# Performance work log

Hardware: AMD Instinct MI355X
Metric: run time of the kernel (lower is better)

Reference implementation:

```python
import jax, jax.numpy as jnp
import numpy as np

XYZ_MIN = jnp.array([-1.0, -1.0, -1.0], dtype=jnp.float32)
XYZ_MAX = jnp.array([1.0, 1.0, 1.0], dtype=jnp.float32)
ACT_SHIFT = float(np.log(1.0 / (1.0 - 1e-6) - 1.0))  # density bias shift
WS = 100  # world_size per axis for num_voxels=1024000 in [-1,1]^3
R, P = 4096, 128  # rays, points per ray


def grid_sample_3d(grid, xyz):
    """Trilinear grid_sample, align_corners=True, zeros padding.
    grid: [C, D, H, W] (D=z, H=y, W=x); xyz: [N, 3] world coords. Returns [N, C]."""
    C, D, H, W = grid.shape
    norm = (xyz - XYZ_MIN) / (XYZ_MAX - XYZ_MIN) * 2.0 - 1.0  # [-1,1]
    sizes = jnp.array([W, H, D], dtype=norm.dtype)
    pix = (norm + 1.0) * 0.5 * (sizes - 1.0)  # align_corners=True mapping
    p0f = jnp.floor(pix)
    frac = pix - p0f
    p0 = p0f.astype(jnp.int32)
    out = jnp.zeros((xyz.shape[0], C), dtype=grid.dtype)
    for dx in (0, 1):
        for dy in (0, 1):
            for dz in (0, 1):
                ix, iy, iz = p0[:, 0] + dx, p0[:, 1] + dy, p0[:, 2] + dz
                wx = frac[:, 0] if dx else 1.0 - frac[:, 0]
                wy = frac[:, 1] if dy else 1.0 - frac[:, 1]
                wz = frac[:, 2] if dz else 1.0 - frac[:, 2]
                valid = ((ix >= 0) & (ix < W) & (iy >= 0) & (iy < H)
                         & (iz >= 0) & (iz < D))
                ixc = jnp.clip(ix, 0, W - 1)
                iyc = jnp.clip(iy, 0, H - 1)
                izc = jnp.clip(iz, 0, D - 1)
                vals = grid[:, izc, iyc, ixc].T  # [N, C]
                out = out + vals * (wx * wy * wz * valid)[:, None]
    return out


def setup_inputs() -> dict:
    key = jax.random.key(0)
    ks = jax.random.split(key, 12)
    origins = jax.random.uniform(ks[0], (R, 3), jnp.float32, -0.5, 0.5)
    directions = jax.random.normal(ks[1], (R, 3), jnp.float32)
    lengths = jax.random.uniform(ks[2], (R, P), jnp.float32, 0.05, 0.6)
    grid_density = jax.random.normal(ks[3], (1, WS, WS, WS), jnp.float32) * 0.1
    grid_color = jax.random.normal(ks[4], (12, WS, WS, WS), jnp.float32) * 0.1
    d_in = 12 + 27
    w1 = jax.random.normal(ks[5], (d_in, 128), jnp.float32) / np.sqrt(d_in)
    b1 = jnp.zeros((128,), jnp.float32)
    w2 = jax.random.normal(ks[6], (128, 128), jnp.float32) / np.sqrt(128)
    b2 = jnp.zeros((128,), jnp.float32)
    w3 = jax.random.normal(ks[7], (128, 3), jnp.float32) / np.sqrt(128)
    b3 = jnp.zeros((3,), jnp.float32)
    return dict(origins=origins, directions=directions, lengths=lengths,
                grid_density=grid_density, grid_color=grid_color,
                w1=w1, b1=b1, w2=w2, b2=b2, w3=w3, b3=b3)


def reference(origins, directions, lengths, grid_density, grid_color,
              w1, b1, w2, b2, w3, b3):
    # ray points: [R, P, 3]
    pts = origins[:, None, :] + directions[:, None, :] * lengths[:, :, None]
    flat = pts.reshape(-1, 3)
    # density branch
    density = grid_sample_3d(grid_density, flat).reshape(R, P, 1)
    interval = jnp.linalg.norm(directions, axis=-1)[:, None, None]
    alpha = 1.0 - (1.0 + jnp.exp(density + ACT_SHIFT)) ** (-interval)
    # color branch: 12-ch feature grid + view-dir PE + small MLP
    color = grid_sample_3d(grid_color, flat).reshape(R, P, 12)
    freqs = jnp.array([1.0, 2.0, 4.0, 8.0], dtype=jnp.float32)
    emb = (directions[:, :, None] * freqs).reshape(R, 12)
    emb = jnp.concatenate([directions, jnp.sin(emb), jnp.cos(emb)], -1)  # [R,27]
    emb = jnp.broadcast_to(emb[:, None, :], (R, P, 27))
    h = jnp.concatenate([color, emb], -1)  # [R,P,39]
    h = jax.nn.relu(h @ w1 + b1)
    h = jax.nn.relu(h @ w2 + b2)
    rgb = jax.nn.sigmoid(h @ w3 + b3)
    return alpha, rgb
```

## Files before the change

kernel.cpp:

```cpp
#include <hip/hip_runtime.h>
#include <hip/hip_bf16.h>
#include <math.h>


typedef __bf16 bf16x4 __attribute__((ext_vector_type(4)));
typedef __bf16 bf16x8 __attribute__((ext_vector_type(8)));
typedef float  f32x4  __attribute__((ext_vector_type(4)));

#define ACT_SHIFT_F (-13.815509557964774f)

#define B1R_B   45056
#define PACK2_B 2142208
#define NEED_FULL 34142208ull

#define EMB_B   53248
#define PACK_B  315392
#define NEED_PACK 32315392ull

__global__ __launch_bounds__(256)
void dvgo_prep2(const float* __restrict__ g_gd, const float* __restrict__ g_gc,
                const float* __restrict__ g_w1, const float* __restrict__ g_w2,
                const float* __restrict__ g_w3, const float* __restrict__ g_dir,
                const float* __restrict__ g_b1,
                bf16x8* __restrict__ pack, __bf16* __restrict__ wsb,
                float* __restrict__ b1r)
{
    const int bid = blockIdx.x;
    const int tid = threadIdx.x;
    if (bid < 3907) {
        const int gi = bid * 256 + tid;
        if (gi >= 1000000) return;
        bf16x8 v0, v1;
        #pragma unroll
        for (int c = 0; c < 8; ++c) v0[c] = (__bf16)g_gc[c * 1000000 + gi];
        #pragma unroll
        for (int c = 0; c < 4; ++c) v1[c] = (__bf16)g_gc[(8 + c) * 1000000 + gi];
        v1[4] = (__bf16)g_gd[gi];
        v1[5] = (__bf16)0.0f; v1[6] = (__bf16)0.0f; v1[7] = (__bf16)0.0f;
        pack[gi * 2 + 0] = v0;
        pack[gi * 2 + 1] = v1;
        return;
    }
    const int idx2 = bid - 3907;
    if (idx2 < 88) {
        const int idx = idx2 * 256 + tid;
        if (idx < 4096) {
            const int j = idx & 7, lane = (idx >> 3) & 63, ct = idx >> 9;
            const int n = ct * 16 + (lane & 15);
            const int k = ((lane >> 4) & 3) * 8 + j;
            wsb[idx] = (__bf16)((k < 12) ? g_w1[k * 128 + n] : 0.0f);
        } else if (idx < 20480) {
            const int i2 = idx - 4096;
            const int j = i2 & 7, lane = (i2 >> 3) & 63, ks = (i2 >> 9) & 3, ct = i2 >> 11;
            const int n = ct * 16 + (lane & 15);
            const int k = ks * 32 + ((lane >> 4) & 3) * 8 + j;
            wsb[idx] = (__bf16)g_w2[k * 128 + n];
        } else if (idx < 22528) {
            const int i3 = idx - 20480;
            const int j = i3 & 7, lane = (i3 >> 3) & 63, ks = i3 >> 9;
            const int c = lane & 15;
            const int k = ks * 32 + ((lane >> 4) & 3) * 8 + j;
            wsb[idx] = (__bf16)((c < 3) ? g_w3[k * 3 + c] : 0.0f);
        }
        return;
    }
    const int rr  = idx2 - 88;
    const int ray = rr * 2 + (tid >> 7);
    const int n   = tid & 127;
    const float d0 = g_dir[ray*3+0], d1 = g_dir[ray*3+1], d2 = g_dir[ray*3+2];
    float s = g_b1[n];
    s += d0 * g_w1[12*128 + n] + d1 * g_w1[13*128 + n] + d2 * g_w1[14*128 + n];
    #pragma unroll
    for (int m = 0; m < 12; ++m) {
        const int i = m >> 2, j = m & 3;
        const float di = (i == 0) ? d0 : ((i == 1) ? d1 : d2);
        const float a = di * (float)(1 << j);
        s += sinf(a) * g_w1[(15 + m)*128 + n];
        s += cosf(a) * g_w1[(27 + m)*128 + n];
    }
    b1r[ray*128 + n] = s;
}

__global__ __launch_bounds__(256, 4)
void dvgo_mlp(const bf16x8* __restrict__ wf, const float* __restrict__ b1r,
              const bf16x8* __restrict__ pack,
              const float* __restrict__ g_org, const float* __restrict__ g_dir,
              const float* __restrict__ g_len,
              const float* __restrict__ g_b2, const float* __restrict__ g_b3,
              float* __restrict__ out_alpha, float* __restrict__ out_rgb)
{
    __shared__ __align__(16) char smem[32768];
    const int tid  = threadIdx.x;
    const int ray  = blockIdx.x;
    const int lane = tid & 63;
    const int wid  = tid >> 6;
    const int lr   = lane & 15;
    const int lk   = lane >> 4;
    const int sz   = (lr & 7) << 4;
    char* slab = smem + wid*8192;

    {
        const int p    = wid*32 + (lane & 31);
        const int dzv  = lane >> 5;
        const float d0 = g_dir[ray*3+0], d1 = g_dir[ray*3+1], d2 = g_dir[ray*3+2];
        const float o0 = g_org[ray*3+0], o1 = g_org[ray*3+1], o2 = g_org[ray*3+2];
        const float len = g_len[ray*128 + p];

        const float px = (o0 + d0*len + 1.0f) * 49.5f;
        const float py = (o1 + d1*len + 1.0f) * 49.5f;
        const float pz = (o2 + d2*len + 1.0f) * 49.5f;
        const float fx = floorf(px), fy = floorf(py), fz = floorf(pz);
        const int ix = (int)fx, iy = (int)fy, iz0 = (int)fz;
        const float qx = px - fx, qy = py - fy, qz = pz - fz;
        const float wxa[2] = {1.0f - qx, qx};
        const float wya[2] = {1.0f - qy, qy};
        const int  cxa[2] = {min(max(ix,0),99),   min(max(ix+1,0),99)};
        const int  cya[2] = {min(max(iy,0),99),   min(max(iy+1,0),99)};
        const bool vxa[2] = {(unsigned)ix < 100u, (unsigned)(ix+1) < 100u};
        const bool vya[2] = {(unsigned)iy < 100u, (unsigned)(iy+1) < 100u};
        const int  iz = iz0 + dzv;
        const float wz = dzv ? qz : (1.0f - qz);
        const int  cz = min(max(iz,0),99);
        const bool vz = (unsigned)iz < 100u;

        float den = 0.0f;
        float cc[12];
        #pragma unroll
        for (int c = 0; c < 12; ++c) cc[c] = 0.0f;

        #pragma unroll
        for (int dy = 0; dy < 2; ++dy)
        #pragma unroll
        for (int dx = 0; dx < 2; ++dx) {
            float w = wxa[dx] * wya[dy] * wz;
            if (!(vxa[dx] && vya[dy] && vz)) w = 0.0f;
            const int gi = (cz*100 + cya[dy])*100 + cxa[dx];
            const bf16x8 v0 = pack[gi*2 + 0];
            const bf16x8 v1 = pack[gi*2 + 1];
            #pragma unroll
            for (int c = 0; c < 8; ++c) cc[c]     += w * (float)v0[c];
            #pragma unroll
            for (int c = 0; c < 4; ++c) cc[8 + c] += w * (float)v1[c];
            den += w * (float)v1[4];
        }

        #pragma unroll
        for (int c = 0; c < 12; ++c) cc[c] += __shfl_xor(cc[c], 32);
        den += __shfl_xor(den, 32);

        if (dzv == 0) {
            const float interval = sqrtf(d0*d0 + d1*d1 + d2*d2);
            const float e = expf(den + ACT_SHIFT_F);
            out_alpha[ray*128 + p] = -expm1f(-interval * log1pf(e));
            bf16x8 f0, f1;
            #pragma unroll
            for (int c = 0; c < 8; ++c) f0[c] = (__bf16)cc[c];
            #pragma unroll
            for (int c = 0; c < 4; ++c) f1[c] = (__bf16)cc[8 + c];
            #pragma unroll
            for (int c = 4; c < 8; ++c) f1[c] = (__bf16)0.0f;
            *(bf16x8*)(slab + (lane & 31)*32 +  0) = f0;
            *(bf16x8*)(slab + (lane & 31)*32 + 16) = f1;
        }
    }

    bf16x8 zed;
    #pragma unroll
    for (int j = 0; j < 8; ++j) zed[j] = (__bf16)0.0f;
    bf16x8 bb[2];
    #pragma unroll
    for (int q = 0; q < 2; ++q) {
        const bf16x8 t = *(const bf16x8*)(slab + (q*16 + lr)*32 + (lk & 1)*16);
        bb[q] = (lk < 2) ? t : zed;
    }

    const int rowb = (wid*32 + lr)*256;
    int rb2[4];
    #pragma unroll
    for (int ks = 0; ks < 4; ++ks)
        rb2[ks] = rowb + ((ks*64 + lk*16) ^ sz);

    #pragma unroll
    for (int ct = 0; ct < 8; ++ct) {
        const bf16x8 aw = wf[ct*64 + lane];
        f32x4 a0 = (f32x4){0.f,0.f,0.f,0.f};
        f32x4 a1 = (f32x4){0.f,0.f,0.f,0.f};
        a0 = __builtin_amdgcn_mfma_f32_16x16x32_bf16(aw, bb[0], a0, 0, 0, 0);
        a1 = __builtin_amdgcn_mfma_f32_16x16x32_bf16(aw, bb[1], a1, 0, 0, 0);
        const f32x4 b1v = *(const f32x4*)(b1r + ray*128 + ct*16 + lk*4);
        bf16x4 h0, h1;
        #pragma unroll
        for (int r = 0; r < 4; ++r) {
            h0[r] = (__bf16)fmaxf(a0[r] + b1v[r], 0.0f);
            h1[r] = (__bf16)fmaxf(a1[r] + b1v[r], 0.0f);
        }
        const int csw = (ct*32 + lk*8) ^ sz;
        *(bf16x4*)(smem + rowb + csw) = h0;
        *(bf16x4*)(smem + rowb + 4096 + csw) = h1;
    }

    bf16x8 hq[2][4];
    #pragma unroll
    for (int q = 0; q < 2; ++q)
        #pragma unroll
        for (int ks = 0; ks < 4; ++ks)
            hq[q][ks] = *(const bf16x8*)(smem + rb2[ks] + q*4096);

    #pragma unroll
    for (int ct = 0; ct < 8; ++ct) {
        bf16x8 aw2[4];
        #pragma unroll
        for (int ks = 0; ks < 4; ++ks)
            aw2[ks] = wf[512 + (ct*4 + ks)*64 + lane];
        f32x4 a0 = (f32x4){0.f,0.f,0.f,0.f};
        f32x4 a1 = (f32x4){0.f,0.f,0.f,0.f};
        #pragma unroll
        for (int ks = 0; ks < 4; ++ks) {
            a0 = __builtin_amdgcn_mfma_f32_16x16x32_bf16(aw2[ks], hq[0][ks], a0, 0, 0, 0);
            a1 = __builtin_amdgcn_mfma_f32_16x16x32_bf16(aw2[ks], hq[1][ks], a1, 0, 0, 0);
        }
        const f32x4 b2v = *(const f32x4*)(g_b2 + ct*16 + lk*4);
        bf16x4 h0, h1;
        #pragma unroll
        for (int r = 0; r < 4; ++r) {
            h0[r] = (__bf16)fmaxf(a0[r] + b2v[r], 0.0f);
            h1[r] = (__bf16)fmaxf(a1[r] + b2v[r], 0.0f);
        }
        const int csw = (ct*32 + lk*8) ^ sz;
        *(bf16x4*)(smem + rowb + csw) = h0;
        *(bf16x4*)(smem + rowb + 4096 + csw) = h1;
    }

    bf16x8 aw3[4];
    #pragma unroll
    for (int ks = 0; ks < 4; ++ks) aw3[ks] = wf[2560 + ks*64 + lane];
    f32x4 acc3[2];
    acc3[0] = (f32x4){0.f,0.f,0.f,0.f};
    acc3[1] = (f32x4){0.f,0.f,0.f,0.f};
    #pragma unroll
    for (int q = 0; q < 2; ++q)
        #pragma unroll
        for (int ks = 0; ks < 4; ++ks) {
            const bf16x8 hq3 = *(const bf16x8*)(smem + rb2[ks] + q*4096);
            acc3[q] = __builtin_amdgcn_mfma_f32_16x16x32_bf16(aw3[ks], hq3, acc3[q], 0, 0, 0);
        }

    float* smf = (float*)slab;
    if (lk == 0) {
        const float b30 = g_b3[0], b31 = g_b3[1], b32 = g_b3[2];
        #pragma unroll
        for (int q = 0; q < 2; ++q) {
            const int o = (q*16 + lr)*3;
            smf[o + 0] = 1.0f / (1.0f + __expf(-(acc3[q][0] + b30)));
            smf[o + 1] = 1.0f / (1.0f + __expf(-(acc3[q][1] + b31)));
            smf[o + 2] = 1.0f / (1.0f + __expf(-(acc3[q][2] + b32)));
        }
    }
    asm volatile("s_waitcnt lgkmcnt(0)");
    __builtin_amdgcn_sched_barrier(0);
    {
        const int base = (ray*128 + wid*32)*3;
        out_rgb[base + lane] = smf[lane];
        if (lane < 32) out_rgb[base + 64 + lane] = smf[64 + lane];
    }
}

__global__ __launch_bounds__(256)
void dvgo_prep_fb(const float* __restrict__ g_gd, const float* __restrict__ g_gc,
                  const float* __restrict__ g_w1, const float* __restrict__ g_w2,
                  const float* __restrict__ g_w3, const float* __restrict__ g_dir,
                  bf16x8* __restrict__ pack, __bf16* __restrict__ wsb, int wbase)
{
    const int bid = blockIdx.x;
    if (bid < wbase) {
        const int gi = bid * 256 + threadIdx.x;
        if (gi >= 1000000) return;
        bf16x8 v0, v1;
        #pragma unroll
        for (int c = 0; c < 8; ++c) v0[c] = (__bf16)g_gc[c * 1000000 + gi];
        #pragma unroll
        for (int c = 0; c < 4; ++c) v1[c] = (__bf16)g_gc[(8 + c) * 1000000 + gi];
        v1[4] = (__bf16)g_gd[gi];
        v1[5] = (__bf16)0.0f; v1[6] = (__bf16)0.0f; v1[7] = (__bf16)0.0f;
        pack[gi * 2 + 0] = v0;
        pack[gi * 2 + 1] = v1;
        return;
    }
    const int idx = (bid - wbase) * 256 + threadIdx.x;
    if (idx < 8192) {
        const int j = idx & 7, lane = (idx >> 3) & 63, ks = (idx >> 9) & 1, ct = idx >> 10;
        const int n = ct * 16 + (lane & 15);
        const int k = ks * 32 + ((lane >> 4) & 3) * 8 + j;
        wsb[idx] = (__bf16)((k < 39) ? g_w1[k * 128 + n] : 0.0f);
    } else if (idx < 24576) {
        const int i2 = idx - 8192;
        const int j = i2 & 7, lane = (i2 >> 3) & 63, ks = (i2 >> 9) & 3, ct = i2 >> 11;
        const int n = ct * 16 + (lane & 15);
        const int k = ks * 32 + ((lane >> 4) & 3) * 8 + j;
        wsb[idx] = (__bf16)g_w2[k * 128 + n];
    }
}

#define FB_FEAT_OFF 0
#define FB_PCC_OFF  16384
#define FB_H1_OFF   0
#define FB_PRGB_OFF 0

template <bool PACKED>
__global__ __launch_bounds__(256, 4)
void dvgo_main(const float* __restrict__ g_org, const float* __restrict__ g_dir,
               const float* __restrict__ g_len, const float* __restrict__ g_gd,
               const float* __restrict__ g_gc, const float* __restrict__ g_b1,
               const float* __restrict__ g_b2, const float* __restrict__ g_w3,
               const float* __restrict__ g_b3, const bf16x8* __restrict__ wf,
               const bf16x8* __restrict__ g_pack,
               float* __restrict__ out_alpha, float* __restrict__ out_rgb)
{
    __shared__ __align__(16) char smem[32768];
    float* smf = (float*)smem;
    const int tid = threadIdx.x;
    const int ray = blockIdx.x;
    const float d0 = g_dir[ray*3+0], d1 = g_dir[ray*3+1], d2 = g_dir[ray*3+2];
    {
        const float o0 = g_org[ray*3+0], o1 = g_org[ray*3+1], o2 = g_org[ray*3+2];
        const int p = tid & 127;
        const int dzv = tid >> 7;
        const float len = g_len[ray*128 + p];
        const float px = (o0 + d0*len + 1.0f) * 49.5f;
        const float py = (o1 + d1*len + 1.0f) * 49.5f;
        const float pz = (o2 + d2*len + 1.0f) * 49.5f;
        const float fx = floorf(px), fy = floorf(py), fz = floorf(pz);
        const int ix = (int)fx, iy = (int)fy, iz0 = (int)fz;
        const float qx = px - fx, qy = py - fy, qz = pz - fz;
        const float wxa[2] = {1.0f - qx, qx};
        const float wya[2] = {1.0f - qy, qy};
        const int  cxa[2] = {min(max(ix,0),99),   min(max(ix+1,0),99)};
        const int  cya[2] = {min(max(iy,0),99),   min(max(iy+1,0),99)};
        const bool vxa[2] = {(unsigned)ix < 100u, (unsigned)(ix+1) < 100u};
        const bool vya[2] = {(unsigned)iy < 100u, (unsigned)(iy+1) < 100u};
        const int  iz = iz0 + dzv;
        const float wz = dzv ? qz : (1.0f - qz);
        const int  cz = min(max(iz,0),99);
        const bool vz = (unsigned)iz < 100u;
        float den = 0.0f;
        float cc[12];
        #pragma unroll
        for (int c = 0; c < 12; ++c) cc[c] = 0.0f;
        #pragma unroll
        for (int dy = 0; dy < 2; ++dy)
        #pragma unroll
        for (int dx = 0; dx < 2; ++dx) {
            float w = wxa[dx] * wya[dy] * wz;
            if (!(vxa[dx] && vya[dy] && vz)) w = 0.0f;
            const int gi = (cz*100 + cya[dy])*100 + cxa[dx];
            if (PACKED) {
                const bf16x8 v0 = g_pack[gi*2 + 0];
                const bf16x8 v1 = g_pack[gi*2 + 1];
                #pragma unroll
                for (int c = 0; c < 8; ++c) cc[c]     += w * (float)v0[c];
                #pragma unroll
                for (int c = 0; c < 4; ++c) cc[8 + c] += w * (float)v1[c];
                den += w * (float)v1[4];
            } else {
                den += w * g_gd[gi];
                #pragma unroll
                for (int c = 0; c < 12; ++c) cc[c] += w * g_gc[c*1000000 + gi];
            }
        }
        if (dzv) {
            #pragma unroll
            for (int c = 0; c < 12; ++c) smf[FB_PCC_OFF/4 + p*13 + c] = cc[c];
            smf[FB_PCC_OFF/4 + p*13 + 12] = den;
        }
        __syncthreads();
        if (!dzv) {
            #pragma unroll
            for (int c = 0; c < 12; ++c) cc[c] += smf[FB_PCC_OFF/4 + p*13 + c];
            den += smf[FB_PCC_OFF/4 + p*13 + 12];
            const float interval = sqrtf(d0*d0 + d1*d1 + d2*d2);
            const float e = expf(den + ACT_SHIFT_F);
            out_alpha[ray*128 + p] = -expm1f(-interval * log1pf(e));
            bf16x8 f0; bf16x4 f1;
            #pragma unroll
            for (int c = 0; c < 8; ++c) f0[c] = (__bf16)cc[c];
            #pragma unroll
            for (int c = 0; c < 4; ++c) f1[c] = (__bf16)cc[8+c];
            const int swz = (p & 7) << 4;
            *reinterpret_cast<bf16x8*>(smem + ((FB_FEAT_OFF + p*128 +  0) ^ swz)) = f0;
            *reinterpret_cast<bf16x4*>(smem + ((FB_FEAT_OFF + p*128 + 16) ^ swz)) = f1;
        } else {
            float vals[52];
            vals[0] = d0; vals[1] = d1; vals[2] = d2;
            #pragma unroll
            for (int i = 0; i < 3; ++i) {
                const float di = (i == 0) ? d0 : ((i == 1) ? d1 : d2);
                #pragma unroll
                for (int j = 0; j < 4; ++j) {
                    const float a = di * (float)(1 << j);
                    vals[3  + i*4 + j] = sinf(a);
                    vals[15 + i*4 + j] = cosf(a);
                }
            }
            #pragma unroll
            for (int c = 27; c < 52; ++c) vals[c] = 0.0f;
            const int swz = (p & 7) << 4;
            #pragma unroll
            for (int i = 0; i < 13; ++i) {
                bf16x4 v4;
                #pragma unroll
                for (int r = 0; r < 4; ++r) v4[r] = (__bf16)vals[i*4 + r];
                *reinterpret_cast<bf16x4*>(smem + ((FB_FEAT_OFF + p*128 + 24 + i*8) ^ swz)) = v4;
            }
        }
    }
    __syncthreads();
    const int lane = tid & 63;
    const int wid  = tid >> 6;
    const int lr   = lane & 15;
    const int lk   = lane >> 4;
    {
        bf16x8 bf[2][2];
        #pragma unroll
        for (int rt = 0; rt < 2; ++rt)
            #pragma unroll
            for (int ks = 0; ks < 2; ++ks) {
                const int pt = wid*32 + rt*16 + lr;
                int a = FB_FEAT_OFF + pt*128 + ks*64 + lk*16; a ^= (pt & 7) << 4;
                bf[rt][ks] = *reinterpret_cast<const bf16x8*>(smem + a);
            }
        __syncthreads();
        f32x4 acc1[2][8];
        #pragma unroll
        for (int rt = 0; rt < 2; ++rt)
            #pragma unroll
            for (int ct = 0; ct < 8; ++ct) acc1[rt][ct] = (f32x4){0.f,0.f,0.f,0.f};
        #pragma unroll
        for (int ct = 0; ct < 8; ++ct) {
            const bf16x8 aw0 = wf[(ct*2 + 0)*64 + lane];
            const bf16x8 aw1 = wf[(ct*2 + 1)*64 + lane];
            #pragma unroll
            for (int rt = 0; rt < 2; ++rt) {
                acc1[rt][ct] = __builtin_amdgcn_mfma_f32_16x16x32_bf16(aw0, bf[rt][0], acc1[rt][ct], 0, 0, 0);
                acc1[rt][ct] = __builtin_amdgcn_mfma_f32_16x16x32_bf16(aw1, bf[rt][1], acc1[rt][ct], 0, 0, 0);
            }
        }
        #pragma unroll
        for (int ct = 0; ct < 8; ++ct) {
            const f32x4 b1v = *reinterpret_cast<const f32x4*>(g_b1 + ct*16 + lk*4);
            #pragma unroll
            for (int rt = 0; rt < 2; ++rt) {
                const int pt = wid*32 + rt*16 + lr;
                bf16x4 hv;
                #pragma unroll
                for (int r = 0; r < 4; ++r)
                    hv[r] = (__bf16)fmaxf(acc1[rt][ct][r] + b1v[r], 0.0f);
                int a = FB_H1_OFF + pt*256 + ct*32 + lk*8; a ^= (pt & 7) << 4;
                *reinterpret_cast<bf16x4*>(smem + a) = hv;
            }
        }
    }
    __syncthreads();
    const int wr = wid >> 1, wc = wid & 1;
    f32x4 acc2[4][4];
    #pragma unroll
    for (int rt = 0; rt < 4; ++rt)
        #pragma unroll
        for (int ct = 0; ct < 4; ++ct) acc2[rt][ct] = (f32x4){0.f,0.f,0.f,0.f};
    #pragma unroll
    for (int ks = 0; ks < 4; ++ks) {
        bf16x8 a2[4];
        #pragma unroll
        for (int rt = 0; rt < 4; ++rt) {
            const int pt = wr*64 + rt*16 + lr;
            int a = FB_H1_OFF + pt*256 + ks*64 + lk*16; a ^= (pt & 7) << 4;
            a2[rt] = *reinterpret_cast<const bf16x8*>(smem + a);
        }
        #pragma unroll
        for (int ct = 0; ct < 4; ++ct) {
            const int ctg = wc*4 + ct;
            const bf16x8 b2f = wf[1024 + (ctg*4 + ks)*64 + lane];
            #pragma unroll
            for (int rt = 0; rt < 4; ++rt)
                acc2[rt][ct] = __builtin_amdgcn_mfma_f32_16x16x32_bf16(a2[rt], b2f, acc2[rt][ct], 0, 0, 0);
        }
    }
    __syncthreads();
    {
        float b2v[4], w30[4], w31[4], w32[4];
        #pragma unroll
        for (int ct = 0; ct < 4; ++ct) {
            const int n2 = wc*64 + ct*16 + lr;
            b2v[ct] = g_b2[n2];
            w30[ct] = g_w3[n2*3 + 0];
            w31[ct] = g_w3[n2*3 + 1];
            w32[ct] = g_w3[n2*3 + 2];
        }
        #pragma unroll
        for (int rt = 0; rt < 4; ++rt)
            #pragma unroll
            for (int r = 0; r < 4; ++r) {
                float s0 = 0.f, s1 = 0.f, s2 = 0.f;
                #pragma unroll
                for (int ct = 0; ct < 4; ++ct) {
                    const float v = fmaxf(acc2[rt][ct][r] + b2v[ct], 0.0f);
                    s0 = fmaf(v, w30[ct], s0);
                    s1 = fmaf(v, w31[ct], s1);
                    s2 = fmaf(v, w32[ct], s2);
                }
                #pragma unroll
                for (int off = 1; off < 16; off <<= 1) {
                    s0 += __shfl_xor(s0, off);
                    s1 += __shfl_xor(s1, off);
                    s2 += __shfl_xor(s2, off);
                }
                if (lr == 0) {
                    const int pt = wr*64 + rt*16 + lk*4 + r;
                    const int base = FB_PRGB_OFF/4 + (wc*128 + pt)*3;
                    smf[base + 0] = s0;
                    smf[base + 1] = s1;
                    smf[base + 2] = s2;
                }
            }
    }
    __syncthreads();
    if (tid < 128) {
        const int p = tid;
        const float s0 = smf[p*3 + 0] + smf[(128 + p)*3 + 0] + g_b3[0];
        const float s1 = smf[p*3 + 1] + smf[(128 + p)*3 + 1] + g_b3[1];
        const float s2 = smf[p*3 + 2] + smf[(128 + p)*3 + 2] + g_b3[2];
        const int pt = ray*128 + p;
        out_rgb[pt*3 + 0] = 1.0f / (1.0f + expf(-s0));
        out_rgb[pt*3 + 1] = 1.0f / (1.0f + expf(-s1));
        out_rgb[pt*3 + 2] = 1.0f / (1.0f + expf(-s2));
    }
}

extern "C" void kernel_launch(void* const* d_in, const int* in_sizes, int n_in,
                              void* d_out, int out_size, void* d_ws, size_t ws_size,
                              hipStream_t stream)
{
    const float* g_org = (const float*)d_in[0];
    const float* g_dir = (const float*)d_in[1];
    const float* g_len = (const float*)d_in[2];
    const float* g_gd  = (const float*)d_in[3];
    const float* g_gc  = (const float*)d_in[4];
    const float* g_w1  = (const float*)d_in[5];
    const float* g_b1  = (const float*)d_in[6];
    const float* g_w2  = (const float*)d_in[7];
    const float* g_b2  = (const float*)d_in[8];
    const float* g_w3  = (const float*)d_in[9];
    const float* g_b3  = (const float*)d_in[10];
    float* out = (float*)d_out;

    if (ws_size >= NEED_FULL) {
        __bf16* wsb  = (__bf16*)d_ws;
        float*  b1r  = (float*)((char*)d_ws + B1R_B);
        bf16x8* pack = (bf16x8*)((char*)d_ws + PACK2_B);
        dvgo_prep2<<<6043, 256, 0, stream>>>(g_gd, g_gc, g_w1, g_w2, g_w3, g_dir,
                                             g_b1, pack, wsb, b1r);
        dvgo_mlp<<<4096, 256, 0, stream>>>((const bf16x8*)wsb, b1r, pack,
                                           g_org, g_dir, g_len,
                                           g_b2, g_b3, out, out + 4096*128);
    } else if (ws_size >= NEED_PACK) {
        __bf16* wsb  = (__bf16*)d_ws;
        bf16x8* pack = (bf16x8*)((char*)d_ws + EMB_B);
        dvgo_prep_fb<<<4011, 256, 0, stream>>>(g_gd, g_gc, g_w1, g_w2, g_w3, g_dir,
                                               pack, wsb, 3907);
        dvgo_main<true><<<4096, 256, 0, stream>>>(g_org, g_dir, g_len, g_gd, g_gc,
                                                  g_b1, g_b2, g_w3, g_b3,
                                                  (const bf16x8*)wsb, pack,
                                                  out, out + 4096*128);
    } else {
        __bf16* wsb = (__bf16*)d_ws;
        dvgo_prep_fb<<<104, 256, 0, stream>>>(g_gd, g_gc, g_w1, g_w2, g_w3, g_dir,
                                              (bf16x8*)d_ws, wsb, 0);
        dvgo_main<false><<<4096, 256, 0, stream>>>(g_org, g_dir, g_len, g_gd, g_gc,
                                                   g_b1, g_b2, g_w3, g_b3,
                                                   (const bf16x8*)wsb, nullptr,
                                                   out, out + 4096*128);
    }
}
```

Measured before the change: 70.15 us.

## Process two rays per block and prefetch second ray's gather during first MLP

Each block now handles two rays. The trilinear gather loads for the second ray are issued before the first ray's MLP runs, and consumed afterward. This is meant to hide gather memory latency behind MFMA work, and it halves the grid size. The cost is more live registers to hold the prefetched loads, which could cause spills or lower occupancy.

```diff
diff --git a/kernel.cpp b/kernel.cpp
--- a/kernel.cpp
+++ b/kernel.cpp
@@ -81,88 +81,91 @@
     b1r[ray*128 + n] = s;
 }
 
-__global__ __launch_bounds__(256, 4)
-void dvgo_mlp(const bf16x8* __restrict__ wf, const float* __restrict__ b1r,
-              const bf16x8* __restrict__ pack,
-              const float* __restrict__ g_org, const float* __restrict__ g_dir,
-              const float* __restrict__ g_len,
-              const float* __restrict__ g_b2, const float* __restrict__ g_b3,
-              float* __restrict__ out_alpha, float* __restrict__ out_rgb)
-{
-    __shared__ __align__(16) char smem[32768];
-    const int tid  = threadIdx.x;
-    const int ray  = blockIdx.x;
-    const int lane = tid & 63;
-    const int wid  = tid >> 6;
-    const int lr   = lane & 15;
-    const int lk   = lane >> 4;
-    const int sz   = (lr & 7) << 4;
-    char* slab = smem + wid*8192;
-
-    {
-        const int p    = wid*32 + (lane & 31);
-        const int dzv  = lane >> 5;
-        const float d0 = g_dir[ray*3+0], d1 = g_dir[ray*3+1], d2 = g_dir[ray*3+2];
-        const float o0 = g_org[ray*3+0], o1 = g_org[ray*3+1], o2 = g_org[ray*3+2];
-        const float len = g_len[ray*128 + p];
-
-        const float px = (o0 + d0*len + 1.0f) * 49.5f;
-        const float py = (o1 + d1*len + 1.0f) * 49.5f;
-        const float pz = (o2 + d2*len + 1.0f) * 49.5f;
-        const float fx = floorf(px), fy = floorf(py), fz = floorf(pz);
-        const int ix = (int)fx, iy = (int)fy, iz0 = (int)fz;
-        const float qx = px - fx, qy = py - fy, qz = pz - fz;
-        const float wxa[2] = {1.0f - qx, qx};
-        const float wya[2] = {1.0f - qy, qy};
-        const int  cxa[2] = {min(max(ix,0),99),   min(max(ix+1,0),99)};
-        const int  cya[2] = {min(max(iy,0),99),   min(max(iy+1,0),99)};
-        const bool vxa[2] = {(unsigned)ix < 100u, (unsigned)(ix+1) < 100u};
-        const bool vya[2] = {(unsigned)iy < 100u, (unsigned)(iy+1) < 100u};
-        const int  iz = iz0 + dzv;
-        const float wz = dzv ? qz : (1.0f - qz);
-        const int  cz = min(max(iz,0),99);
-        const bool vz = (unsigned)iz < 100u;
-
-        float den = 0.0f;
-        float cc[12];
-        #pragma unroll
-        for (int c = 0; c < 12; ++c) cc[c] = 0.0f;
-
-        #pragma unroll
-        for (int dy = 0; dy < 2; ++dy)
+struct GLoads { bf16x8 v[8]; float w[4]; };
+
+__device__ __forceinline__ void gather_issue(
+    const bf16x8* __restrict__ pack,
+    const float* __restrict__ g_org, const float* __restrict__ g_dir,
+    const float* __restrict__ g_len, int ray, int p, int dzv, GLoads& G)
+{
+    const float d0 = g_dir[ray*3+0], d1 = g_dir[ray*3+1], d2 = g_dir[ray*3+2];
+    const float o0 = g_org[ray*3+0], o1 = g_org[ray*3+1], o2 = g_org[ray*3+2];
+    const float len = g_len[ray*128 + p];
+    const float px = (o0 + d0*len + 1.0f) * 49.5f;
+    const float py = (o1 + d1*len + 1.0f) * 49.5f;
+    const float pz = (o2 + d2*len + 1.0f) * 49.5f;
+    const float fx = floorf(px), fy = floorf(py), fz = floorf(pz);
+    const int ix = (int)fx, iy = (int)fy, iz0 = (int)fz;
+    const float qx = px - fx, qy = py - fy, qz = pz - fz;
+    const float wxa[2] = {1.0f - qx, qx};
+    const float wya[2] = {1.0f - qy, qy};
+    const int  cxa[2] = {min(max(ix,0),99),   min(max(ix+1,0),99)};
+    const int  cya[2] = {min(max(iy,0),99),   min(max(iy+1,0),99)};
+    const bool vxa[2] = {(unsigned)ix < 100u, (unsigned)(ix+1) < 100u};
+    const bool vya[2] = {(unsigned)iy < 100u, (unsigned)(iy+1) < 100u};
+    const int  iz = iz0 + dzv;
+    const float wz = dzv ? qz : (1.0f - qz);
+    const int  cz = min(max(iz,0),99);
+    const bool vz = (unsigned)iz < 100u;
+    #pragma unroll
+    for (int dy = 0; dy < 2; ++dy)
         #pragma unroll
         for (int dx = 0; dx < 2; ++dx) {
+            const int i = dy*2 + dx;
             float w = wxa[dx] * wya[dy] * wz;
             if (!(vxa[dx] && vya[dy] && vz)) w = 0.0f;
             const int gi = (cz*100 + cya[dy])*100 + cxa[dx];
-            const bf16x8 v0 = pack[gi*2 + 0];
-            const bf16x8 v1 = pack[gi*2 + 1];
-            #pragma unroll
-            for (int c = 0; c < 8; ++c) cc[c]     += w * (float)v0[c];
-            #pragma unroll
-            for (int c = 0; c < 4; ++c) cc[8 + c] += w * (float)v1[c];
-            den += w * (float)v1[4];
-        }
-
-        #pragma unroll
-        for (int c = 0; c < 12; ++c) cc[c] += __shfl_xor(cc[c], 32);
-        den += __shfl_xor(den, 32);
-
-        if (dzv == 0) {
-            const float interval = sqrtf(d0*d0 + d1*d1 + d2*d2);
-            const float e = expf(den + ACT_SHIFT_F);
-            out_alpha[ray*128 + p] = -expm1f(-interval * log1pf(e));
-            bf16x8 f0, f1;
-            #pragma unroll
-            for (int c = 0; c < 8; ++c) f0[c] = (__bf16)cc[c];
-            #pragma unroll
-            for (int c = 0; c < 4; ++c) f1[c] = (__bf16)cc[8 + c];
-            #pragma unroll
-            for (int c = 4; c < 8; ++c) f1[c] = (__bf16)0.0f;
-            *(bf16x8*)(slab + (lane & 31)*32 +  0) = f0;
-            *(bf16x8*)(slab + (lane & 31)*32 + 16) = f1;
-        }
-    }
+            G.v[i*2 + 0] = pack[gi*2 + 0];
+            G.v[i*2 + 1] = pack[gi*2 + 1];
+            G.w[i] = w;
+        }
+}
+
+__device__ __forceinline__ void gather_consume(
+    const GLoads& G, const float* __restrict__ g_dir,
+    int ray, int p, int dzv, float* __restrict__ out_alpha, char* slab, int lane)
+{
+    float den = 0.0f;
+    float cc[12];
+    #pragma unroll
+    for (int c = 0; c < 12; ++c) cc[c] = 0.0f;
+    #pragma unroll
+    for (int i = 0; i < 4; ++i) {
+        const float w = G.w[i];
+        #pragma unroll
+        for (int c = 0; c < 8; ++c) cc[c]     += w * (float)G.v[i*2 + 0][c];
+        #pragma unroll
+        for (int c = 0; c < 4; ++c) cc[8 + c] += w * (float)G.v[i*2 + 1][c];
+        den += w * (float)G.v[i*2 + 1][4];
+    }
+    #pragma unroll
+    for (int c = 0; c < 12; ++c) cc[c] += __shfl_xor(cc[c], 32);
+    den += __shfl_xor(den, 32);
+
+    if (dzv == 0) {
+        const float d0 = g_dir[ray*3+0], d1 = g_dir[ray*3+1], d2 = g_dir[ray*3+2];
+        const float interval = sqrtf(d0*d0 + d1*d1 + d2*d2);
+        const float e = expf(den + ACT_SHIFT_F);
+        out_alpha[ray*128 + p] = -expm1f(-interval * log1pf(e));
+        bf16x8 f0, f1;
+        #pragma unroll
+        for (int c = 0; c < 8; ++c) f0[c] = (__bf16)cc[c];
+        #pragma unroll
+        for (int c = 0; c < 4; ++c) f1[c] = (__bf16)cc[8 + c];
+        #pragma unroll
+        for (int c = 4; c < 8; ++c) f1[c] = (__bf16)0.0f;
+        *(bf16x8*)(slab + (lane & 31)*32 +  0) = f0;
+        *(bf16x8*)(slab + (lane & 31)*32 + 16) = f1;
+    }
+}
+
+__device__ __forceinline__ void mlp_one(
+    const bf16x8* __restrict__ wf, const float* __restrict__ b1r,
+    const float* __restrict__ g_b2, const float* __restrict__ g_b3,
+    float* __restrict__ out_rgb, char* smem, char* slab,
+    int ray, int lane, int wid, int lr, int lk, int sz)
+{
+    const int rowb = (wid*32 + lr)*256;
 
     bf16x8 zed;
     #pragma unroll
@@ -173,12 +176,6 @@
         const bf16x8 t = *(const bf16x8*)(slab + (q*16 + lr)*32 + (lk & 1)*16);
         bb[q] = (lk < 2) ? t : zed;
     }
-
-    const int rowb = (wid*32 + lr)*256;
-    int rb2[4];
-    #pragma unroll
-    for (int ks = 0; ks < 4; ++ks)
-        rb2[ks] = rowb + ((ks*64 + lk*16) ^ sz);
 
     #pragma unroll
     for (int ct = 0; ct < 8; ++ct) {
@@ -204,7 +201,7 @@
     for (int q = 0; q < 2; ++q)
         #pragma unroll
         for (int ks = 0; ks < 4; ++ks)
-            hq[q][ks] = *(const bf16x8*)(smem + rb2[ks] + q*4096);
+            hq[q][ks] = *(const bf16x8*)(smem + rowb + ((ks*64 + lk*16) ^ sz) + q*4096);
 
     #pragma unroll
     for (int ct = 0; ct < 8; ++ct) {
@@ -241,7 +238,7 @@
     for (int q = 0; q < 2; ++q)
         #pragma unroll
         for (int ks = 0; ks < 4; ++ks) {
-            const bf16x8 hq3 = *(const bf16x8*)(smem + rb2[ks] + q*4096);
+            const bf16x8 hq3 = *(const bf16x8*)(smem + rowb + ((ks*64 + lk*16) ^ sz) + q*4096);
             acc3[q] = __builtin_amdgcn_mfma_f32_16x16x32_bf16(aw3[ks], hq3, acc3[q], 0, 0, 0);
         }
 
@@ -263,6 +260,40 @@
         out_rgb[base + lane] = smf[lane];
         if (lane < 32) out_rgb[base + 64 + lane] = smf[64 + lane];
     }
+}
+
+__global__ __launch_bounds__(256, 4)
+void dvgo_mlp(const bf16x8* __restrict__ wf, const float* __restrict__ b1r,
+              const bf16x8* __restrict__ pack,
+              const float* __restrict__ g_org, const float* __restrict__ g_dir,
+              const float* __restrict__ g_len,
+              const float* __restrict__ g_b2, const float* __restrict__ g_b3,
+              float* __restrict__ out_alpha, float* __restrict__ out_rgb)
+{
+    __shared__ __align__(16) char smem[32768];
+    const int tid  = threadIdx.x;
+    const int rayA = blockIdx.x * 2;
+    const int rayB = rayA + 1;
+    const int lane = tid & 63;
+    const int wid  = tid >> 6;
+    const int lr   = lane & 15;
+    const int lk   = lane >> 4;
+    const int sz   = (lr & 7) << 4;
+    const int p    = wid*32 + (lane & 31);
+    const int dzv  = lane >> 5;
+    char* slab = smem + wid*8192;
+
+    GLoads GA;
+    gather_issue(pack, g_org, g_dir, g_len, rayA, p, dzv, GA);
+    gather_consume(GA, g_dir, rayA, p, dzv, out_alpha, slab, lane);
+
+    GLoads GB;
+    gather_issue(pack, g_org, g_dir, g_len, rayB, p, dzv, GB);
+
+    mlp_one(wf, b1r, g_b2, g_b3, out_rgb, smem, slab, rayA, lane, wid, lr, lk, sz);
+
+    gather_consume(GB, g_dir, rayB, p, dzv, out_alpha, slab, lane);
+    mlp_one(wf, b1r, g_b2, g_b3, out_rgb, smem, slab, rayB, lane, wid, lr, lk, sz);
 }
 
 __global__ __launch_bounds__(256)
@@ -558,7 +589,7 @@
         bf16x8* pack = (bf16x8*)((char*)d_ws + PACK2_B);
         dvgo_prep2<<<6043, 256, 0, stream>>>(g_gd, g_gc, g_w1, g_w2, g_w3, g_dir,
                                              g_b1, pack, wsb, b1r);
-        dvgo_mlp<<<4096, 256, 0, stream>>>((const bf16x8*)wsb, b1r, pack,
+        dvgo_mlp<<<2048, 256, 0, stream>>>((const bf16x8*)wsb, b1r, pack,
                                            g_org, g_dir, g_len,
                                            g_b2, g_b3, out, out + 4096*128);
     } else if (ws_size >= NEED_PACK) {
```

After: 109.3 us. +55.7%, slower.
